# Kernel optimization log

Measured on AMD Instinct MI355X. Metric: run time of the kernel, lower is better.

Reference implementation:

```python
import jax, jax.numpy as jnp
import numpy as np
from jax import lax

WINDOW_SIZE = 11
SIGMA = 1.5
C1 = 0.01 ** 2
C2 = 0.03 ** 2


def _make_window():
    xs = np.arange(WINDOW_SIZE) - WINDOW_SIZE // 2
    g = np.exp(-(xs.astype(np.float32) ** 2) / (2.0 * SIGMA ** 2))
    g = g / g.sum()
    w2d = np.outer(g, g).astype(np.float32)  # (ws, ws)
    return jnp.asarray(w2d)[None, None, :, :]  # (O=1, I=1, ws, ws)


def _blur(x, window):
    pad = WINDOW_SIZE // 2
    return lax.conv_general_dilated(
        x, window,
        window_strides=(1, 1),
        padding=[(pad, pad), (pad, pad)],
        dimension_numbers=("NCHW", "OIHW", "NCHW"),
    )


def setup_inputs() -> dict:
    key = jax.random.key(0)
    k1, k2 = jax.random.split(key)
    shape = (64, 1, 512, 512)
    img1 = jax.random.uniform(k1, shape, dtype=jnp.float32)
    img2 = jax.random.uniform(k2, shape, dtype=jnp.float32)
    return {"img1": img1, "img2": img2}


def reference(img1, img2):
    window = _make_window()
    mu1 = _blur(img1, window)
    mu2 = _blur(img2, window)
    mu1_sq = mu1 * mu1
    mu2_sq = mu2 * mu2
    mu1_mu2 = mu1 * mu2
    sigma1_sq = _blur(img1 * img1, window) - mu1_sq
    sigma2_sq = _blur(img2 * img2, window) - mu2_sq
    sigma12 = _blur(img1 * img2, window) - mu1_mu2
    ssim_map = ((2.0 * mu1_mu2 + C1) * (2.0 * sigma12 + C2)) / (
        (mu1_sq + mu2_sq + C1) * (sigma1_sq + sigma2_sq + C2)
    )
    return ssim_map.mean()  # size_average=True
```

## Files before the change

kernel.cpp:

```cpp
#include <hip/hip_runtime.h>

#define IMG 512
#define HALO 5
#define BAND 16
#define NB 8
#define RING 26

#define W0 1.0283800e-03f
#define W1 7.5987582e-03f
#define W2 3.6000773e-02f
#define W3 1.0936070e-01f
#define W4 2.1300553e-01f
#define W5 2.6601172e-01f

typedef float f2 __attribute__((ext_vector_type(2)));

__device__ __forceinline__ f2 pkfma(f2 a, f2 b, f2 c) {
    return __builtin_elementwise_fma(a, b, c);
}

#define LGKM_BARRIER() asm volatile("s_waitcnt lgkmcnt(0)\n\ts_barrier" ::: "memory")

__global__ __launch_bounds__(256, 4)
void ssim_main(const float* __restrict__ img1, const float* __restrict__ img2,
               float* __restrict__ part)
{
    const float Wt[11] = {W0,W1,W2,W3,W4,W5,W4,W3,W2,W1,W0};
    constexpr float C1 = 1.0e-4f;
    constexpr float C2 = 9.0e-4f;

    __shared__ float4 sH[RING][64];
    __shared__ float  sRed[4];

    const int bx      = blockIdx.x;
    const int n       = bx >> 5;
    const int stripe  = (bx >> 2) & 7;
    const int quarter = bx & 3;
    const int gx0     = stripe << 6;
    const int base    = quarter << 7;
    const int tid     = threadIdx.x;
    const bool edge   = (stripe == 0) | (stripe == 7);

    const float* __restrict__ base1 = img1 + (size_t)n * IMG * IMG;
    const float* __restrict__ base2 = img2 + (size_t)n * IMG * IMG;

    float acc = 0.0f;

    auto loadRowP = [&](const float* r1, const float* r2, bool rok, int gcb_,
                        float4* px, float4* py) {
        #pragma unroll
        for (int t = 0; t < 5; ++t) {
            int gc = gcb_ - 8 + (t << 2);
            bool ok = rok && (gc >= 0) && (gc < IMG);
            px[t] = ok ? ((const float4*)r1)[t] : make_float4(0.f,0.f,0.f,0.f);
            py[t] = ok ? ((const float4*)r2)[t] : make_float4(0.f,0.f,0.f,0.f);
        }
    };

    auto hblurRegs = [&](const float4* px, const float4* py, f2* m, f2* t2) {
        #pragma unroll
        for (int o = 0; o < 4; ++o) { m[o] = f2{0.f,0.f}; t2[o] = f2{0.f,0.f}; }
        #pragma unroll
        for (int t = 0; t < 5; ++t) {
            #pragma unroll
            for (int e = 0; e < 4; ++e) {
                const int j = (t << 2) + e;
                if (j < 3 || j > 16) continue;
                const float x = (e==0) ? px[t].x : (e==1) ? px[t].y : (e==2) ? px[t].z : px[t].w;
                const float y = (e==0) ? py[t].x : (e==1) ? py[t].y : (e==2) ? py[t].z : py[t].w;
                const f2 v  = {x, y};
                const f2 s2 = {fmaf(x, x, y*y), x*y};
                #pragma unroll
                for (int o = 0; o < 4; ++o) {
                    const int k = j - 3 - o;
                    if (0 <= k && k <= 10) {
                        const f2 w = {Wt[k], Wt[k]};
                        m[o]  = pkfma(w, v,  m[o]);
                        t2[o] = pkfma(w, s2, t2[o]);
                    }
                }
            }
        }
    };

    auto horizStore = [&](const float4* px, const float4* py, int slot, int cg) {
        f2 m[4], t2[4];
        hblurRegs(px, py, m, t2);
        const int c4 = cg << 2;
        #pragma unroll
        for (int o = 0; o < 4; ++o) {
            const int wc = (c4 + o) ^ cg;
            sH[slot][wc] = make_float4(m[o].x, m[o].y, t2[o].x, t2[o].y);
        }
    };

    const int rr  = tid >> 4;
    const int cgs = tid & 15;
    const int gcb = gx0 + (cgs << 2);

    const float* p1 = base1 + (ptrdiff_t)(base + 21 + rr) * IMG + gcb - 8;
    const float* p2 = base2 + (ptrdiff_t)(base + 21 + rr) * IMG + gcb - 8;

    float4 px[5], py[5];
    f2 bm[4], bt[4];

    auto loadSteady = [&](int k) {
        const bool rowsafe = (quarter < 3) | (k < NB - 2);
        if (rowsafe & (!edge)) {
            #pragma unroll
            for (int t = 0; t < 5; ++t) {
                px[t] = ((const float4*)p1)[t];
                py[t] = ((const float4*)p2)[t];
            }
        } else {
            const int gr = base + (k << 4) + 21 + rr;
            loadRowP(p1, p2, (unsigned)gr < (unsigned)IMG, gcb, px, py);
        }
        p1 += BAND * IMG;
        p2 += BAND * IMG;
    };

    const int col  = tid & 63;
    const int rcol = col ^ (col >> 2);
    const int wv   = __builtin_amdgcn_readfirstlane(tid >> 6);

    auto vertical = [&](int sb_) {
        const int d0 = sb_ + (wv << 2);
        f2 ma[4] = {f2{0.f,0.f},f2{0.f,0.f},f2{0.f,0.f},f2{0.f,0.f}};
        f2 sa[4] = {f2{0.f,0.f},f2{0.f,0.f},f2{0.f,0.f},f2{0.f,0.f}};
        #pragma unroll
        for (int i = 0; i < 14; ++i) {
            int s = d0 + i;
            s -= (s >= RING) ? RING : 0;
            const float4 q = sH[s][rcol];
            const f2 v = {q.x, q.y};
            const f2 u = {q.z, q.w};
            #pragma unroll
            for (int o = 0; o < 4; ++o) {
                const int k = i - o;
                if (0 <= k && k <= 10) {
                    const f2 w = {Wt[k], Wt[k]};
                    ma[o] = pkfma(w, v, ma[o]);
                    sa[o] = pkfma(w, u, sa[o]);
                }
            }
        }
        #pragma unroll
        for (int o = 0; o < 4; ++o) {
            const f2 m   = ma[o];
            const f2 tt  = sa[o];
            const f2 msq = m * m;
            const float mu12  = m.x * m.y;
            const float musum = msq.x + msq.y;
            const float g12 = tt.y - mu12;
            const float gs  = tt.x - musum;
            const float num = fmaf(2.f, mu12, C1) * fmaf(2.f, g12, C2);
            const float den = (musum + C1) * (gs + C2);
            acc = fmaf(num, __builtin_amdgcn_rcpf(den), acc);
        }
    };

    loadSteady(0);

    for (int task = tid; task < RING * 16; task += 256) {
        const int i   = task >> 4;
        const int cg  = task & 15;
        const int gr  = base - HALO + i;
        const int gcb2 = gx0 + (cg << 2);
        const float* r1 = base1 + (ptrdiff_t)gr * IMG + gcb2 - 8;
        const float* r2 = base2 + (ptrdiff_t)gr * IMG + gcb2 - 8;
        float4 qx[5], qy[5];
        if (!edge && gr >= 0) {
            #pragma unroll
            for (int t = 0; t < 5; ++t) {
                qx[t] = ((const float4*)r1)[t];
                qy[t] = ((const float4*)r2)[t];
            }
        } else {
            loadRowP(r1, r2, gr >= 0, gcb2, qx, qy);
        }
        horizStore(qx, qy, i, cg);
    }

    int sb = 0;
    for (int b = 0; b < NB; ++b) {
        if (b <= NB - 2) {
            hblurRegs(px, py, bm, bt);
            if (b <= NB - 3)
                loadSteady(b + 1);
        }

        LGKM_BARRIER();
        vertical(sb);
        LGKM_BARRIER();

        if (b <= NB - 2) {
            int t = sb + rr;
            t -= (t >= RING) ? RING : 0;
            const int c4 = cgs << 2;
            #pragma unroll
            for (int o = 0; o < 4; ++o) {
                const int wc = (c4 + o) ^ cgs;
                sH[t][wc] = make_float4(bm[o].x, bm[o].y, bt[o].x, bt[o].y);
            }
        }
        sb += BAND; sb -= (sb >= RING) ? RING : 0;
    }

    #pragma unroll
    for (int off = 32; off > 0; off >>= 1)
        acc += __shfl_down(acc, off, 64);
    if ((tid & 63) == 0) sRed[tid >> 6] = acc;
    LGKM_BARRIER();
    if (tid == 0) part[bx] = sRed[0] + sRed[1] + sRed[2] + sRed[3];
}

__global__ void ssim_finalize(const float* __restrict__ part, float* __restrict__ out)
{
    __shared__ double sD[4];
    double s = 0.0;
    const int t = threadIdx.x;
    for (int i = t; i < 2048; i += 256) s += (double)part[i];
    #pragma unroll
    for (int off = 32; off > 0; off >>= 1)
        s += __shfl_down(s, off, 64);
    if ((t & 63) == 0) sD[t >> 6] = s;
    __syncthreads();
    if (t == 0) out[0] = (float)((sD[0] + sD[1] + sD[2] + sD[3]) * (1.0 / 16777216.0));
}

extern "C" void kernel_launch(void* const* d_in, const int* in_sizes, int n_in,
                              void* d_out, int out_size, void* d_ws, size_t ws_size,
                              hipStream_t stream)
{
    const float* img1 = (const float*)d_in[0];
    const float* img2 = (const float*)d_in[1];
    float* out  = (float*)d_out;
    float* part = (float*)d_ws;

    ssim_main<<<2048, 256, 0, stream>>>(img1, img2, part);
    ssim_finalize<<<1, 256, 0, stream>>>(part, out);
}
```

Baseline: 176.7 us.

## Load next band in-iteration and pin packed blur weights in registers

Restructures the band loop so each iteration issues global loads for the next row band before the vertical pass, then does the horizontal blur after the barrier instead of holding a blurred result across iterations. This removes the two-stage register pipeline (raw prefetch plus blurred band) to reduce register pressure. Weights are also materialized once as packed f2 registers behind an empty asm to keep them in VGPRs rather than rematerialized constants. The trade-off is less latency hiding, since the horizontal blur now waits on loads issued in the same iteration, plus 22 extra VGPRs for weights.

```diff
diff --git a/kernel.cpp b/kernel.cpp
--- a/kernel.cpp
+++ b/kernel.cpp
@@ -25,9 +25,16 @@
 void ssim_main(const float* __restrict__ img1, const float* __restrict__ img2,
                float* __restrict__ part)
 {
-    const float Wt[11] = {W0,W1,W2,W3,W4,W5,W4,W3,W2,W1,W0};
     constexpr float C1 = 1.0e-4f;
     constexpr float C2 = 9.0e-4f;
+
+    const float Wt[11] = {W0,W1,W2,W3,W4,W5,W4,W3,W2,W1,W0};
+    f2 W2r[11];
+    #pragma unroll
+    for (int k = 0; k < 11; ++k) {
+        W2r[k] = f2{Wt[k], Wt[k]};
+        asm volatile("" : "+v"(W2r[k]));
+    }
 
     __shared__ float4 sH[RING][64];
     __shared__ float  sRed[4];
@@ -57,9 +64,9 @@
         }
     };
 
-    auto hblurRegs = [&](const float4* px, const float4* py, f2* m, f2* t2) {
-        #pragma unroll
-        for (int o = 0; o < 4; ++o) { m[o] = f2{0.f,0.f}; t2[o] = f2{0.f,0.f}; }
+    auto horizStore = [&](const float4* px, const float4* py, int slot, int cg) {
+        f2 m[4]  = {f2{0.f,0.f},f2{0.f,0.f},f2{0.f,0.f},f2{0.f,0.f}};
+        f2 t2[4] = {f2{0.f,0.f},f2{0.f,0.f},f2{0.f,0.f},f2{0.f,0.f}};
         #pragma unroll
         for (int t = 0; t < 5; ++t) {
             #pragma unroll
@@ -74,18 +81,12 @@
                 for (int o = 0; o < 4; ++o) {
                     const int k = j - 3 - o;
                     if (0 <= k && k <= 10) {
-                        const f2 w = {Wt[k], Wt[k]};
-                        m[o]  = pkfma(w, v,  m[o]);
-                        t2[o] = pkfma(w, s2, t2[o]);
+                        m[o]  = pkfma(W2r[k], v,  m[o]);
+                        t2[o] = pkfma(W2r[k], s2, t2[o]);
                     }
                 }
             }
         }
-    };
-
-    auto horizStore = [&](const float4* px, const float4* py, int slot, int cg) {
-        f2 m[4], t2[4];
-        hblurRegs(px, py, m, t2);
         const int c4 = cg << 2;
         #pragma unroll
         for (int o = 0; o < 4; ++o) {
@@ -100,25 +101,6 @@
 
     const float* p1 = base1 + (ptrdiff_t)(base + 21 + rr) * IMG + gcb - 8;
     const float* p2 = base2 + (ptrdiff_t)(base + 21 + rr) * IMG + gcb - 8;
-
-    float4 px[5], py[5];
-    f2 bm[4], bt[4];
-
-    auto loadSteady = [&](int k) {
-        const bool rowsafe = (quarter < 3) | (k < NB - 2);
-        if (rowsafe & (!edge)) {
-            #pragma unroll
-            for (int t = 0; t < 5; ++t) {
-                px[t] = ((const float4*)p1)[t];
-                py[t] = ((const float4*)p2)[t];
-            }
-        } else {
-            const int gr = base + (k << 4) + 21 + rr;
-            loadRowP(p1, p2, (unsigned)gr < (unsigned)IMG, gcb, px, py);
-        }
-        p1 += BAND * IMG;
-        p2 += BAND * IMG;
-    };
 
     const int col  = tid & 63;
     const int rcol = col ^ (col >> 2);
@@ -139,9 +121,8 @@
             for (int o = 0; o < 4; ++o) {
                 const int k = i - o;
                 if (0 <= k && k <= 10) {
-                    const f2 w = {Wt[k], Wt[k]};
-                    ma[o] = pkfma(w, v, ma[o]);
-                    sa[o] = pkfma(w, u, sa[o]);
+                    ma[o] = pkfma(W2r[k], v, ma[o]);
+                    sa[o] = pkfma(W2r[k], u, sa[o]);
                 }
             }
         }
@@ -159,8 +140,6 @@
             acc = fmaf(num, __builtin_amdgcn_rcpf(den), acc);
         }
     };
-
-    loadSteady(0);
 
     for (int task = tid; task < RING * 16; task += 256) {
         const int i   = task >> 4;
@@ -184,25 +163,32 @@
 
     int sb = 0;
     for (int b = 0; b < NB; ++b) {
-        if (b <= NB - 2) {
-            hblurRegs(px, py, bm, bt);
-            if (b <= NB - 3)
-                loadSteady(b + 1);
+        float4 px[5], py[5];
+        const bool pf = (b + 1 < NB);
+        if (pf) {
+            const bool rowsafe = (quarter < 3) | (b < NB - 2);
+            if (rowsafe & (!edge)) {
+                #pragma unroll
+                for (int t = 0; t < 5; ++t) {
+                    px[t] = ((const float4*)p1)[t];
+                    py[t] = ((const float4*)p2)[t];
+                }
+            } else {
+                const int gr = base + (b << 4) + 21 + rr;
+                loadRowP(p1, p2, (unsigned)gr < (unsigned)IMG, gcb, px, py);
+            }
         }
 
         LGKM_BARRIER();
         vertical(sb);
         LGKM_BARRIER();
 
-        if (b <= NB - 2) {
+        if (pf) {
             int t = sb + rr;
             t -= (t >= RING) ? RING : 0;
-            const int c4 = cgs << 2;
-            #pragma unroll
-            for (int o = 0; o < 4; ++o) {
-                const int wc = (c4 + o) ^ cgs;
-                sH[t][wc] = make_float4(bm[o].x, bm[o].y, bt[o].x, bt[o].y);
-            }
+            horizStore(px, py, t, cgs);
+            p1 += BAND * IMG;
+            p2 += BAND * IMG;
         }
         sb += BAND; sb -= (sb >= RING) ? RING : 0;
     }
```

Result: faster. 172.7 us (-2.3%).
